# Kernel optimization log

Hardware: AMD Instinct MI355X
Metric: run time of the kernel (lower is better)

The kernel has to match this reference:

```python
import jax, jax.numpy as jnp
import numpy as np

EMBED_DIM = 512

def setup_inputs() -> dict:
    key = jax.random.key(0)
    ks = jax.random.split(key, 8)
    B, N, M, C = 4, 4096, 4096, EMBED_DIM
    s = 1.0 / np.sqrt(C)
    return {
        "rgb_features": jax.random.normal(ks[0], (B, N, C), jnp.float32),
        "depth_features": jax.random.normal(ks[1], (B, M, C), jnp.float32),
        "Wq": jax.random.normal(ks[2], (C, C), jnp.float32) * s,
        "bq": jnp.zeros((C,), jnp.float32),
        "Wk": jax.random.normal(ks[3], (C, C), jnp.float32) * s,
        "bk": jnp.zeros((C,), jnp.float32),
        "Wv": jax.random.normal(ks[4], (C, C), jnp.float32) * s,
        "bv": jnp.zeros((C,), jnp.float32),
    }

def reference(rgb_features, depth_features, Wq, bq, Wk, bk, Wv, bv):
    C = rgb_features.shape[-1]
    scale = C ** (-0.5)
    Q = rgb_features @ Wq + bq          # [B, N, C]
    K = depth_features @ Wk + bk        # [B, M, C]
    V = depth_features @ Wv + bv        # [B, M, C]
    scores = jnp.einsum('bnc,bmc->bnm', Q, K) * scale
    attn = jax.nn.softmax(scores, axis=-1)
    return jnp.einsum('bnm,bmc->bnc', attn, V)
```

## Files before the change

### kernel.cpp

```cpp
#include <hip/hip_runtime.h>
#include <hip/hip_bf16.h>
#include <stdint.h>


typedef unsigned short u16;
typedef __attribute__((ext_vector_type(8))) short bf16x8;
typedef __attribute__((ext_vector_type(16))) float f32x16;
typedef __attribute__((ext_vector_type(4))) unsigned short u16x4;

#define GLD_LDS16(g, l)                                                        \
  __builtin_amdgcn_global_load_lds(                                            \
      (const __attribute__((address_space(1))) unsigned int*)(g),              \
      (__attribute__((address_space(3))) unsigned int*)(l), 16, 0, 0)

__device__ __forceinline__ u16 f2bf(float f) {
  unsigned x = __float_as_uint(f);
  return (u16)((x + 0x7fffu + ((x >> 16) & 1u)) >> 16);
}
__device__ __forceinline__ float bf2f(short s) {
  return __uint_as_float((unsigned)(unsigned short)s << 16);
}

template <int TM, int TN, int BIAS_MODE, int OUT_MODE, int MINW>
__global__ __launch_bounds__(256, MINW) void gemm32(
    const u16* __restrict__ A, const u16* __restrict__ Bm,
    const float* __restrict__ bias, void* __restrict__ Cv, int M, int N, int K,
    long long sAb, long long sBb, long long sCb, float scale) {
  constexpr int WROWS = TM / 2;
  constexpr int WCOLS = TN / 2;
  constexpr int MSUB = WROWS / 32;
  constexpr int NSUB = WCOLS / 32;
  constexpr int CA = TM / 64;
  constexpr int CB = TN / 64;

  const int bz = blockIdx.z;
  A += (size_t)bz * sAb;
  Bm += (size_t)bz * sBb;

  const int bm = blockIdx.y * TM;
  const int bn = blockIdx.x * TN;

  __shared__ u16 As[2][TM * 32];
  __shared__ u16 Bs[2][TN * 32];

  const int tid = threadIdx.x;
  const int wave = tid >> 6;
  const int lane = tid & 63;
  const int ln31 = lane & 31;
  const int half = lane >> 5;
  const int wr = wave >> 1;
  const int wc = wave & 1;

  const int rowA = lane >> 2;
  const int swz = ((lane & 3) ^ ((rowA + (rowA >> 2)) & 3)) * 8;
  const int gl = (ln31 + (ln31 >> 2)) & 3;

  f32x16 acc[MSUB][NSUB] = {};

  auto stage = [&](int buf, int k0) {
#pragma unroll
    for (int r = 0; r < CA; ++r) {
      const int ch = wave * CA + r;
      GLD_LDS16(A + (size_t)(bm + ch * 16 + rowA) * K + k0 + swz,
                As[buf] + ch * 16 * 32);
    }
#pragma unroll
    for (int r = 0; r < CB; ++r) {
      const int ch = wave * CB + r;
      GLD_LDS16(Bm + (size_t)(bn + ch * 16 + rowA) * K + k0 + swz,
                Bs[buf] + ch * 16 * 32);
    }
  };

  const int niter = K >> 5;
  stage(0, 0);
  for (int it = 0; it < niter; ++it) {
    __syncthreads();
    if (it + 1 < niter) stage((it + 1) & 1, (it + 1) * 32);
    const int buf = it & 1;
#pragma unroll
    for (int kc = 0; kc < 2; ++kc) {
      const int p = ((kc * 2 + half) ^ gl) * 8;
      bf16x8 af[MSUB], bfv[NSUB];
#pragma unroll
      for (int mt = 0; mt < MSUB; ++mt)
        af[mt] =
            *(const bf16x8*)&As[buf][(wr * WROWS + mt * 32 + ln31) * 32 + p];
#pragma unroll
      for (int nt = 0; nt < NSUB; ++nt)
        bfv[nt] =
            *(const bf16x8*)&Bs[buf][(wc * WCOLS + nt * 32 + ln31) * 32 + p];
#pragma unroll
      for (int mt = 0; mt < MSUB; ++mt)
#pragma unroll
        for (int nt = 0; nt < NSUB; ++nt)
          acc[mt][nt] = __builtin_amdgcn_mfma_f32_32x32x16_bf16(
              af[mt], bfv[nt], acc[mt][nt], 0, 0, 0);
    }
  }

  const int crow0 = bm + wr * WROWS + 4 * half;
  const int ccol0 = bn + wc * WCOLS + ln31;
#pragma unroll
  for (int mt = 0; mt < MSUB; ++mt) {
#pragma unroll
    for (int nt = 0; nt < NSUB; ++nt) {
      const int col = ccol0 + nt * 32;
#pragma unroll
      for (int r = 0; r < 16; ++r) {
        const int row = crow0 + mt * 32 + (r & 3) + 8 * (r >> 2);
        float v = acc[mt][nt][r];
        if constexpr (BIAS_MODE == 1) v += bias[col];
        if constexpr (BIAS_MODE == 2) v += bias[row];
        const size_t idx = (size_t)bz * (size_t)sCb + (size_t)row * N + col;
        if constexpr (OUT_MODE == 0)
          ((u16*)Cv)[idx] = f2bf(v);
        else if constexpr (OUT_MODE == 1)
          ((float*)Cv)[idx] = v;
        else
          ((u16*)Cv)[idx] = f2bf(__expf(v * scale));
      }
    }
  }
}

#define XA_STGA(buf, j, k0)                                                    \
  GLD_LDS16(Ag + (size_t)((j) * 32 + (wv & 3) * 8 + (wv >> 2) * 128 + rlane) * \
                    512 +                                                      \
                (k0) + swz8,                                                   \
            &As[buf][((j) * 32 + (wv & 3) * 8 + (wv >> 2) * 128) * 64])
#define XA_STGB(buf, j, k0)                                                    \
  GLD_LDS16(Bg + (size_t)((j) * 64 + wv * 8 + rlane) * 512 + (k0) + swz8,      \
            &Bs[buf][((j) * 64 + wv * 8) * 64])

#define XA_PHASE(F, NV, PFS)                                                   \
  {                                                                            \
    bf16x8 af[4];                                                              \
    {                                                                          \
      const int arow = (wm * 128 + (F) * 32 + ln31) * 64;                      \
      _Pragma("unroll") for (int k = 0; k < 4; ++k) af[k] =                    \
          *(const bf16x8*)&As[p][arow + (((2 * k + half) ^ s7) << 3)];         \
    }                                                                          \
    if ((F) == 0) {                                                            \
      _Pragma("unroll") for (int n = 0; n < 2; ++n) {                          \
        const int brow = (wn * 64 + n * 32 + ln31) * 64;                       \
        _Pragma("unroll") for (int k = 0; k < 4; ++k) bfr[n][k] =              \
            *(const bf16x8*)&Bs[p][brow + (((2 * k + half) ^ s7) << 3)];       \
      }                                                                        \
    }                                                                          \
    PFS;                                                                       \
    __builtin_amdgcn_s_barrier();                                              \
    asm volatile("s_waitcnt lgkmcnt(0)" ::: "memory");                         \
    __builtin_amdgcn_sched_barrier(0);                                         \
    __builtin_amdgcn_s_setprio(1);                                             \
    _Pragma("unroll") for (int k = 0; k < 4; ++k) {                            \
      acc[F][0] = __builtin_amdgcn_mfma_f32_32x32x16_bf16(af[k], bfr[0][k],    \
                                                          acc[F][0], 0, 0, 0); \
      acc[F][1] = __builtin_amdgcn_mfma_f32_32x32x16_bf16(af[k], bfr[1][k],    \
                                                          acc[F][1], 0, 0, 0); \
    }                                                                          \
    __builtin_amdgcn_s_setprio(0);                                             \
    asm volatile("s_waitcnt vmcnt(" NV ")" ::: "memory");                      \
    __builtin_amdgcn_s_barrier();                                              \
    asm volatile("" ::: "memory");                                             \
  }

__global__ __launch_bounds__(512, 2) void gemm256_exp(
    const u16* __restrict__ Qm, const u16* __restrict__ Km,
    u16* __restrict__ Sout, long long sAb, long long sSb, float scale) {
  const int bz = blockIdx.z;
  const int bm = blockIdx.y * 256;
  const int bn = blockIdx.x * 256;
  const u16* Ag = Qm + (size_t)bz * (size_t)sAb + (size_t)bm * 512;
  const u16* Bg = Km + (size_t)bz * (size_t)sAb + (size_t)bn * 512;

  __shared__ u16 As[2][256 * 64];
  __shared__ u16 Bs[2][256 * 64];

  const int tid = threadIdx.x;
  const int wv = tid >> 6;
  const int lane = tid & 63;
  const int ln31 = lane & 31;
  const int half = lane >> 5;
  const int wm = wv >> 2;
  const int wn = wv & 3;
  const int rlane = lane >> 3;
  const int swz8 = ((lane & 7) ^ rlane) << 3;
  const int s7 = ln31 & 7;

  f32x16 acc[4][2] = {};
  bf16x8 bfr[2][4];

#pragma unroll
  for (int j = 0; j < 4; ++j) XA_STGB(0, j, 0);
#pragma unroll
  for (int j = 0; j < 4; ++j) XA_STGA(0, j, 0);
  asm volatile("s_waitcnt vmcnt(3)" ::: "memory");
  __builtin_amdgcn_s_barrier();
  asm volatile("" ::: "memory");

  for (int t = 0; t < 7; ++t) {
    const int p = t & 1;
    const int q = p ^ 1;
    const int kn = (t + 1) << 6;
    XA_PHASE(0, "4", { XA_STGB(q, 0, kn); XA_STGB(q, 1, kn); });
    XA_PHASE(1, "5", { XA_STGB(q, 2, kn); XA_STGB(q, 3, kn); });
    XA_PHASE(2, "6", { XA_STGA(q, 0, kn); XA_STGA(q, 1, kn); });
    XA_PHASE(3, "3", { XA_STGA(q, 2, kn); XA_STGA(q, 3, kn); });
  }
  {
    const int p = 1;
    XA_PHASE(0, "2", {});
    XA_PHASE(1, "1", {});
    XA_PHASE(2, "0", {});
    XA_PHASE(3, "0", {});
  }

  const size_t ob = (size_t)bz * (size_t)sSb;
  const int c0 = bn + wn * 64 + ln31;
  const int r0 = bm + wm * 128 + 4 * half;
#pragma unroll
  for (int m = 0; m < 4; ++m) {
#pragma unroll
    for (int n = 0; n < 2; ++n) {
      const int col = c0 + n * 32;
#pragma unroll
      for (int r = 0; r < 16; ++r) {
        const int row = r0 + m * 32 + (r & 3) + 8 * (r >> 2);
        Sout[ob + (size_t)row * 4096 + col] = f2bf(__expf(acc[m][n][r] * scale));
      }
    }
  }
}

__global__ __launch_bounds__(256, 2) void pv_gemm(
    const u16* __restrict__ P, const u16* __restrict__ Vt,
    float* __restrict__ O) {
  const int bz = blockIdx.z;
  const u16* A = P + (size_t)bz * (4096ull * 4096ull);
  const u16* B = Vt + (size_t)bz * (512ull * 4096ull);
  float* Ob = O + (size_t)bz * (4096ull * 512ull);

  const int bm = blockIdx.y * 64;
  const int bn = blockIdx.x * 256;

  __shared__ u16 As[2][64 * 32];
  __shared__ u16 Bs[2][256 * 32];
  __shared__ float den_s[64];

  const int tid = threadIdx.x;
  const int wave = tid >> 6;
  const int lane = tid & 63;
  const int ln31 = lane & 31;
  const int half = lane >> 5;

  const int rowA = lane >> 2;
  const int swz = ((lane & 3) ^ ((rowA + (rowA >> 2)) & 3)) * 8;
  const int gl = (ln31 + (ln31 >> 2)) & 3;

  f32x16 acc[2][2] = {};
  float rsum[2] = {0.f, 0.f};

  auto stage = [&](int buf, int k0) {
    GLD_LDS16(A + (size_t)(bm + wave * 16 + rowA) * 4096 + k0 + swz,
              As[buf] + wave * 16 * 32);
#pragma unroll
    for (int r = 0; r < 4; ++r) {
      const int ch = wave * 4 + r;
      GLD_LDS16(B + (size_t)(bn + ch * 16 + rowA) * 4096 + k0 + swz,
                Bs[buf] + ch * 16 * 32);
    }
  };

  stage(0, 0);
  for (int it = 0; it < 128; ++it) {
    __syncthreads();
    if (it + 1 < 128) stage((it + 1) & 1, (it + 1) * 32);
    const int buf = it & 1;
#pragma unroll
    for (int kc = 0; kc < 2; ++kc) {
      const int p = ((kc * 2 + half) ^ gl) * 8;
      bf16x8 af[2], bfv[2];
#pragma unroll
      for (int mt = 0; mt < 2; ++mt)
        af[mt] = *(const bf16x8*)&As[buf][(mt * 32 + ln31) * 32 + p];
#pragma unroll
      for (int nt = 0; nt < 2; ++nt)
        bfv[nt] =
            *(const bf16x8*)&Bs[buf][(wave * 64 + nt * 32 + ln31) * 32 + p];
#pragma unroll
      for (int mt = 0; mt < 2; ++mt) {
#pragma unroll
        for (int j = 0; j < 8; ++j) rsum[mt] += bf2f(af[mt][j]);
#pragma unroll
        for (int nt = 0; nt < 2; ++nt)
          acc[mt][nt] = __builtin_amdgcn_mfma_f32_32x32x16_bf16(
              af[mt], bfv[nt], acc[mt][nt], 0, 0, 0);
      }
    }
  }

#pragma unroll
  for (int mt = 0; mt < 2; ++mt) rsum[mt] += __shfl_xor(rsum[mt], 32, 64);
  __syncthreads();
  if (wave == 0 && half == 0) {
    den_s[ln31] = rsum[0];
    den_s[32 + ln31] = rsum[1];
  }
  __syncthreads();

  const int crow0 = 4 * half;
  const int ccol0 = bn + wave * 64 + ln31;
#pragma unroll
  for (int mt = 0; mt < 2; ++mt) {
#pragma unroll
    for (int r = 0; r < 16; ++r) {
      const int rl = crow0 + mt * 32 + (r & 3) + 8 * (r >> 2);
      const float rd = 1.0f / den_s[rl];
#pragma unroll
      for (int nt = 0; nt < 2; ++nt)
        Ob[(size_t)(bm + rl) * 512 + ccol0 + nt * 32] = acc[mt][nt][r] * rd;
    }
  }
}

__global__ __launch_bounds__(256) void cvt_pair(const float* __restrict__ x,
                                                const float* __restrict__ y,
                                                u16* __restrict__ ox,
                                                u16* __restrict__ oy, int n4) {
  const int i = blockIdx.x * 256 + threadIdx.x;
  if (i >= n4) return;
  const float4 a = ((const float4*)x)[i];
  const float4 b = ((const float4*)y)[i];
  u16x4 oa, ob;
  oa[0] = f2bf(a.x); oa[1] = f2bf(a.y); oa[2] = f2bf(a.z); oa[3] = f2bf(a.w);
  ob[0] = f2bf(b.x); ob[1] = f2bf(b.y); ob[2] = f2bf(b.z); ob[3] = f2bf(b.w);
  ((u16x4*)ox)[i] = oa;
  ((u16x4*)oy)[i] = ob;
}

__global__ __launch_bounds__(256) void wtrans_k(const float* __restrict__ W,
                                                u16* __restrict__ WT) {
  const int tr = blockIdx.y * 64;
  const int tc = blockIdx.x * 64;
  __shared__ float T[64][65];
  const int t = threadIdx.x;
  const int r0 = t >> 4;
  const int c0 = (t & 15) * 4;
#pragma unroll
  for (int rr = 0; rr < 4; ++rr) {
    const int row = rr * 16 + r0;
    const float4 w = *(const float4*)&W[(size_t)(tr + row) * 512 + tc + c0];
    T[row][c0 + 0] = w.x; T[row][c0 + 1] = w.y;
    T[row][c0 + 2] = w.z; T[row][c0 + 3] = w.w;
  }
  __syncthreads();
#pragma unroll
  for (int rr = 0; rr < 4; ++rr) {
    const int orow = rr * 16 + r0;
    u16x4 o;
#pragma unroll
    for (int j = 0; j < 4; ++j) o[j] = f2bf(T[c0 + j][orow]);
    *(u16x4*)&WT[(size_t)(tc + orow) * 512 + tr + c0] = o;
  }
}

extern "C" void kernel_launch(void* const* d_in, const int* in_sizes, int n_in,
                              void* d_out, int out_size, void* d_ws,
                              size_t ws_size, hipStream_t stream) {
  const float* rgb = (const float*)d_in[0];
  const float* dep = (const float*)d_in[1];
  const float* Wq = (const float*)d_in[2];
  const float* bq = (const float*)d_in[3];
  const float* Wk = (const float*)d_in[4];
  const float* bk = (const float*)d_in[5];
  const float* Wv = (const float*)d_in[6];
  const float* bv = (const float*)d_in[7];
  float* out = (float*)d_out;

  const int B = 4, N = 4096, M = 4096, C = 512;
  const size_t nBNC = (size_t)B * N * C;
  const float scale = 0.044194173824159216f;

  char* ws = (char*)d_ws;
  size_t off = 0;
  auto carve = [&](size_t bytes) -> void* {
    void* p = ws + off;
    off += (bytes + 255) & ~(size_t)255;
    return p;
  };
  u16* rgb_bf = (u16*)carve(nBNC * 2);
  u16* dep_bf = (u16*)carve(nBNC * 2);
  u16* WqT = (u16*)carve((size_t)C * C * 2);
  u16* WkT = (u16*)carve((size_t)C * C * 2);
  u16* WvT = (u16*)carve((size_t)C * C * 2);
  u16* Qb = (u16*)carve(nBNC * 2);
  u16* Kb = (u16*)carve(nBNC * 2);
  u16* Vt = (u16*)carve(nBNC * 2);
  u16* Sb = (u16*)carve((size_t)B * N * M * 2);

  const long long strQ = (long long)N * C;
  const long long strS = (long long)N * M;
  const long long strV = (long long)C * M;

  cvt_pair<<<8192, 256, 0, stream>>>(rgb, dep, rgb_bf, dep_bf, (int)(nBNC / 4));
  wtrans_k<<<dim3(8, 8), 256, 0, stream>>>(Wq, WqT);
  wtrans_k<<<dim3(8, 8), 256, 0, stream>>>(Wk, WkT);
  wtrans_k<<<dim3(8, 8), 256, 0, stream>>>(Wv, WvT);

  gemm32<128, 128, 1, 0, 4><<<dim3(4, 128, 1), 256, 0, stream>>>(
      rgb_bf, WqT, bq, Qb, 16384, 512, 512, 0, 0, 0, 1.f);
  gemm32<128, 128, 1, 0, 4><<<dim3(4, 128, 1), 256, 0, stream>>>(
      dep_bf, WkT, bk, Kb, 16384, 512, 512, 0, 0, 0, 1.f);
  gemm32<128, 128, 2, 0, 4><<<dim3(32, 4, 4), 256, 0, stream>>>(
      WvT, dep_bf, bv, Vt, 512, 4096, 512, 0, strQ, strV, 1.f);

  gemm256_exp<<<dim3(16, 16, 4), 512, 0, stream>>>(Qb, Kb, Sb, strQ, strS,
                                                   scale);

  pv_gemm<<<dim3(2, 64, 4), 256, 0, stream>>>(Sb, Vt, out);
}
```

Baseline: 377.9 us.

## Deepen PV GEMM pipeline to four stages and compute row sums via MFMA

The PV kernel moves from a double-buffered LDS pipeline with __syncthreads to a four-stage ring. Each stage is guarded by explicit vmcnt waits and raw s_barrier, and MFMA issue is wrapped in setprio. The scalar per-lane bf16 row-sum accumulation and its shuffle/LDS reduction are replaced by an extra MFMA against a ones vector, so the softmax denominator lands directly in accumulator layout. This aims to hide global-load latency and remove VALU work from the inner loop, at the cost of more LDS (about 80KB per block at occupancy 2), extra MFMA work, and reliance on hand-counted vmcnt values.

```diff
diff --git a/kernel.cpp b/kernel.cpp
--- a/kernel.cpp
+++ b/kernel.cpp
@@ -233,6 +233,40 @@
   }
 }
 
+#define PV_BODY(IT, NV, DO_STAGE, DO_TAIL)                                     \
+  {                                                                            \
+    const int buf = (IT) & 3;                                                  \
+    if (DO_STAGE) stage(((IT) + 3) & 3, ((IT) + 3) * 32);                      \
+    bf16x8 af[2][2], bfv[2][2];                                                \
+    _Pragma("unroll") for (int kc = 0; kc < 2; ++kc) {                         \
+      const int p = ((kc * 2 + half) ^ gl) * 8;                                \
+      _Pragma("unroll") for (int mt = 0; mt < 2; ++mt)                         \
+        af[kc][mt] = *(const bf16x8*)&As[buf][(mt * 32 + ln31) * 32 + p];      \
+      _Pragma("unroll") for (int nt = 0; nt < 2; ++nt)                         \
+        bfv[kc][nt] =                                                          \
+            *(const bf16x8*)&Bs[buf][(wave * 64 + nt * 32 + ln31) * 32 + p];   \
+    }                                                                          \
+    __builtin_amdgcn_s_barrier();                                              \
+    asm volatile("s_waitcnt lgkmcnt(0)" ::: "memory");                         \
+    __builtin_amdgcn_sched_barrier(0);                                         \
+    __builtin_amdgcn_s_setprio(1);                                             \
+    _Pragma("unroll") for (int kc = 0; kc < 2; ++kc) {                         \
+      _Pragma("unroll") for (int mt = 0; mt < 2; ++mt) {                       \
+        dacc[mt] = __builtin_amdgcn_mfma_f32_32x32x16_bf16(                    \
+            af[kc][mt], onesv, dacc[mt], 0, 0, 0);                             \
+        _Pragma("unroll") for (int nt = 0; nt < 2; ++nt)                       \
+          acc[mt][nt] = __builtin_amdgcn_mfma_f32_32x32x16_bf16(               \
+              af[kc][mt], bfv[kc][nt], acc[mt][nt], 0, 0, 0);                  \
+      }                                                                        \
+    }                                                                          \
+    __builtin_amdgcn_s_setprio(0);                                             \
+    if (DO_TAIL) {                                                             \
+      asm volatile("s_waitcnt vmcnt(" NV ")" ::: "memory");                    \
+      __builtin_amdgcn_s_barrier();                                            \
+      asm volatile("" ::: "memory");                                           \
+    }                                                                          \
+  }
+
 __global__ __launch_bounds__(256, 2) void pv_gemm(
     const u16* __restrict__ P, const u16* __restrict__ Vt,
     float* __restrict__ O) {
@@ -244,9 +278,8 @@
   const int bm = blockIdx.y * 64;
   const int bn = blockIdx.x * 256;
 
-  __shared__ u16 As[2][64 * 32];
-  __shared__ u16 Bs[2][256 * 32];
-  __shared__ float den_s[64];
+  __shared__ u16 As[4][64 * 32];
+  __shared__ u16 Bs[4][256 * 32];
 
   const int tid = threadIdx.x;
   const int wave = tid >> 6;
@@ -259,7 +292,10 @@
   const int gl = (ln31 + (ln31 >> 2)) & 3;
 
   f32x16 acc[2][2] = {};
-  float rsum[2] = {0.f, 0.f};
+  f32x16 dacc[2] = {};
+  bf16x8 onesv;
+#pragma unroll
+  for (int j = 0; j < 8; ++j) onesv[j] = (short)0x3F80;
 
   auto stage = [&](int buf, int k0) {
     GLD_LDS16(A + (size_t)(bm + wave * 16 + rowA) * 4096 + k0 + swz,
@@ -273,41 +309,16 @@
   };
 
   stage(0, 0);
-  for (int it = 0; it < 128; ++it) {
-    __syncthreads();
-    if (it + 1 < 128) stage((it + 1) & 1, (it + 1) * 32);
-    const int buf = it & 1;
-#pragma unroll
-    for (int kc = 0; kc < 2; ++kc) {
-      const int p = ((kc * 2 + half) ^ gl) * 8;
-      bf16x8 af[2], bfv[2];
-#pragma unroll
-      for (int mt = 0; mt < 2; ++mt)
-        af[mt] = *(const bf16x8*)&As[buf][(mt * 32 + ln31) * 32 + p];
-#pragma unroll
-      for (int nt = 0; nt < 2; ++nt)
-        bfv[nt] =
-            *(const bf16x8*)&Bs[buf][(wave * 64 + nt * 32 + ln31) * 32 + p];
-#pragma unroll
-      for (int mt = 0; mt < 2; ++mt) {
-#pragma unroll
-        for (int j = 0; j < 8; ++j) rsum[mt] += bf2f(af[mt][j]);
-#pragma unroll
-        for (int nt = 0; nt < 2; ++nt)
-          acc[mt][nt] = __builtin_amdgcn_mfma_f32_32x32x16_bf16(
-              af[mt], bfv[nt], acc[mt][nt], 0, 0, 0);
-      }
-    }
-  }
-
-#pragma unroll
-  for (int mt = 0; mt < 2; ++mt) rsum[mt] += __shfl_xor(rsum[mt], 32, 64);
-  __syncthreads();
-  if (wave == 0 && half == 0) {
-    den_s[ln31] = rsum[0];
-    den_s[32 + ln31] = rsum[1];
-  }
-  __syncthreads();
+  stage(1, 32);
+  stage(2, 64);
+  asm volatile("s_waitcnt vmcnt(10)" ::: "memory");
+  __builtin_amdgcn_s_barrier();
+  asm volatile("" ::: "memory");
+
+  for (int it = 0; it < 125; ++it) PV_BODY(it, "10", true, true);
+  PV_BODY(125, "5", false, true);
+  PV_BODY(126, "0", false, true);
+  PV_BODY(127, "0", false, false);
 
   const int crow0 = 4 * half;
   const int ccol0 = bn + wave * 64 + ln31;
@@ -316,7 +327,7 @@
 #pragma unroll
     for (int r = 0; r < 16; ++r) {
       const int rl = crow0 + mt * 32 + (r & 3) + 8 * (r >> 2);
-      const float rd = 1.0f / den_s[rl];
+      const float rd = 1.0f / dacc[mt][r];
 #pragma unroll
       for (int nt = 0; nt < 2; ++nt)
         Ob[(size_t)(bm + rl) * 512 + ccol0 + nt * 32] = acc[mt][nt][r] * rd;
```

Result: slower. 387.3 us (+2.5%).
